# Kernel tuning notes

Measured on AMD Instinct MI355X. Metric: run time of the kernel, lower is better.

Reference implementation:

```python
import jax, jax.numpy as jnp
import numpy as np

EPS = 1e-07
NUM_ITERATIONS = 3

B, O, H, W, I, D = 8, 32, 14, 14, 32, 16


def squash(s, axis=-1):
    # squared norm over capsule dim
    sq = jnp.sum(s * s, axis=axis)                      # [..., ] norms
    safe = jnp.sqrt(sq + EPS)
    factor = sq / (1.0 + sq)
    return (factor / safe)[..., None] * s


def setup_inputs() -> dict:
    key = jax.random.key(0)
    k1, = jax.random.split(key, 1)
    preds = jax.random.normal(k1, (B, O, H, W, I, D), dtype=jnp.float32)
    b = jnp.zeros((1, O, H, W, I), dtype=jnp.float32)   # routing logits param
    return {"tensor_of_prediction_vector": preds, "b": b}


def reference(tensor_of_prediction_vector, b):
    preds = tensor_of_prediction_vector                 # [B,O,H,W,I,D]
    c = jax.nn.softmax(b, axis=-1)                      # [1,O,H,W,I]
    v = squash(jnp.sum(c[..., None] * preds, axis=-2))  # [B,O,H,W,D]
    b_batch = b
    for _ in range(NUM_ITERATIONS):
        # agreement: dot(pred, v) over capsule dim -> [B,O,H,W,I]
        b_batch = b_batch + jnp.sum(preds * v[..., None, :], axis=-1)
        c = jax.nn.softmax(b_batch, axis=-1)
        v = squash(jnp.sum(preds * c[..., None], axis=-2))
    return v
```

## Files before the change

kernel.cpp:

```cpp
#include <hip/hip_runtime.h>


#define EPSQ 1e-7f

constexpr int NI = 32, ND = 16;
constexpr int SITES = 50176;
constexpr int OHW   = 6272;
constexpr int THREADS = 256;
constexpr int BLOCKS  = SITES / 64;

__device__ __forceinline__ float dpp_xor1(float x) {
    return __int_as_float(__builtin_amdgcn_mov_dpp(__float_as_int(x), 0xB1, 0xF, 0xF, true));
}
__device__ __forceinline__ float dpp_xor2(float x) {
    return __int_as_float(__builtin_amdgcn_mov_dpp(__float_as_int(x), 0x4E, 0xF, 0xF, true));
}
__device__ __forceinline__ void fma4(float4& a, float c, const float4& x) {
    a.x = fmaf(c, x.x, a.x); a.y = fmaf(c, x.y, a.y);
    a.z = fmaf(c, x.z, a.z); a.w = fmaf(c, x.w, a.w);
}
__device__ __forceinline__ float dot4(const float4& a, const float4& b) {
    return fmaf(a.x, b.x, fmaf(a.y, b.y, fmaf(a.z, b.z, a.w * b.w)));
}
__device__ __forceinline__ void qred4(float4& a) {
    a.x += dpp_xor1(a.x); a.y += dpp_xor1(a.y);
    a.z += dpp_xor1(a.z); a.w += dpp_xor1(a.w);
    a.x += dpp_xor2(a.x); a.y += dpp_xor2(a.y);
    a.z += dpp_xor2(a.z); a.w += dpp_xor2(a.w);
}

__global__ __launch_bounds__(256, 2) void routing_kernel(
    const float* __restrict__ preds,
    const float* __restrict__ bparam,
    float* __restrict__ out)
{
    __shared__ float4 lds4[4096];
    const int tid  = threadIdx.x;
    const int lane = tid & 63;
    const int wib  = tid >> 6;
    const int wave = blockIdx.x * 4 + wib;
    const int q    = lane & 3;
    const int s_w  = lane >> 2;
    const int site = wave * 16 + s_w;

    float4* wlds = lds4 + wib * 1024;
    const float4* pg = (const float4*)preds + (size_t)wave * 2048;

    float4 t0[16], t1[16];
    #pragma unroll
    for (int k = 0; k < 16; ++k) t0[k] = pg[k * 64 + lane];
    #pragma unroll
    for (int k = 0; k < 16; ++k) t1[k] = pg[1024 + k * 64 + lane];

    const int sohw = site % OHW;
    const float4* bb4 = (const float4*)(bparam + (size_t)sohw * NI + q * 8);
    const float4 bA = bb4[0], bB = bb4[1];
    float bl[8] = {bA.x, bA.y, bA.z, bA.w, bB.x, bB.y, bB.z, bB.w};

    float4 p[8][4];
    const int cb = 32 * q;

    #pragma unroll
    for (int k = 0; k < 16; ++k) {
        const int x = k >> 1;
        wlds[x * 128 + ((((k & 1) * 64) + lane) ^ x)] = t0[k];
    }
    asm volatile("s_waitcnt lgkmcnt(0)" ::: "memory");
    if (s_w < 8) {
        const int x = s_w;
        #pragma unroll
        for (int r = 0; r < 8; ++r)
            #pragma unroll
            for (int u = 0; u < 4; ++u)
                p[r][u] = wlds[x * 128 + ((cb + 4 * r + u) ^ x)];
    }
    asm volatile("s_waitcnt lgkmcnt(0)" ::: "memory");
    #pragma unroll
    for (int k = 0; k < 16; ++k) {
        const int x = k >> 1;
        wlds[x * 128 + ((((k & 1) * 64) + lane) ^ x)] = t1[k];
    }
    asm volatile("s_waitcnt lgkmcnt(0)" ::: "memory");
    if (s_w >= 8) {
        const int x = s_w - 8;
        #pragma unroll
        for (int r = 0; r < 8; ++r)
            #pragma unroll
            for (int u = 0; u < 4; ++u)
                p[r][u] = wlds[x * 128 + ((cb + 4 * r + u) ^ x)];
    }

    float4 v0, v1, v2, v3;

    auto pass = [&]() {
        float e[8];
        float sm = 0.0f;
        #pragma unroll
        for (int k = 0; k < 8; ++k) { e[k] = __expf(bl[k]); sm += e[k]; }
        sm += dpp_xor1(sm);
        sm += dpp_xor2(sm);
        const float r = __frcp_rn(sm);

        float4 s0 = {0,0,0,0}, s1 = {0,0,0,0}, s2 = {0,0,0,0}, s3 = {0,0,0,0};
        #pragma unroll
        for (int k = 0; k < 8; ++k) {
            fma4(s0, e[k], p[k][0]); fma4(s1, e[k], p[k][1]);
            fma4(s2, e[k], p[k][2]); fma4(s3, e[k], p[k][3]);
        }
        qred4(s0); qred4(s1); qred4(s2); qred4(s3);

        const float sqt = dot4(s0, s0) + dot4(s1, s1) + dot4(s2, s2) + dot4(s3, s3);
        const float sq  = r * r * sqt;
        const float f   = sq * __frcp_rn(1.0f + sq) * __frsqrt_rn(sq + EPSQ) * r;
        v0.x = f*s0.x; v0.y = f*s0.y; v0.z = f*s0.z; v0.w = f*s0.w;
        v1.x = f*s1.x; v1.y = f*s1.y; v1.z = f*s1.z; v1.w = f*s1.w;
        v2.x = f*s2.x; v2.y = f*s2.y; v2.z = f*s2.z; v2.w = f*s2.w;
        v3.x = f*s3.x; v3.y = f*s3.y; v3.z = f*s3.z; v3.w = f*s3.w;
    };

    pass();

    #pragma unroll
    for (int it = 0; it < 3; ++it) {
        #pragma unroll
        for (int k = 0; k < 8; ++k) {
            bl[k] += dot4(p[k][0], v0) + dot4(p[k][1], v1)
                   + dot4(p[k][2], v2) + dot4(p[k][3], v3);
        }
        pass();
    }

    float4 w = (q == 0) ? v0 : (q == 1) ? v1 : (q == 2) ? v2 : v3;
    ((float4*)out)[(size_t)site * 4 + q] = w;
}

extern "C" void kernel_launch(void* const* d_in, const int* in_sizes, int n_in,
                              void* d_out, int out_size, void* d_ws, size_t ws_size,
                              hipStream_t stream) {
    const float* preds  = (const float*)d_in[0];
    const float* bparam = (const float*)d_in[1];
    float* out = (float*)d_out;
    routing_kernel<<<BLOCKS, THREADS, 0, stream>>>(preds, bparam, out);
}
```

Baseline: 27.64 us.

## Split each site across eight lanes to cut registers and raise occupancy

Result: slower. 32.50 us (+17.6%).

```diff
diff --git a/kernel.cpp b/kernel.cpp
--- a/kernel.cpp
+++ b/kernel.cpp
@@ -2,18 +2,25 @@
 
 
 #define EPSQ 1e-7f
+#define LOG2E 1.442695041f
 
 constexpr int NI = 32, ND = 16;
 constexpr int SITES = 50176;
 constexpr int OHW   = 6272;
 constexpr int THREADS = 256;
-constexpr int BLOCKS  = SITES / 64;
+constexpr int BLOCKS  = SITES / 32;
 
-__device__ __forceinline__ float dpp_xor1(float x) {
+__device__ __forceinline__ float dpp1(float x) {
     return __int_as_float(__builtin_amdgcn_mov_dpp(__float_as_int(x), 0xB1, 0xF, 0xF, true));
 }
-__device__ __forceinline__ float dpp_xor2(float x) {
+__device__ __forceinline__ float dpp2(float x) {
     return __int_as_float(__builtin_amdgcn_mov_dpp(__float_as_int(x), 0x4E, 0xF, 0xF, true));
+}
+__device__ __forceinline__ float dpp4(float x) {
+    return __int_as_float(__builtin_amdgcn_mov_dpp(__float_as_int(x), 0x141, 0xF, 0xF, true));
+}
+__device__ __forceinline__ float red8(float x) {
+    x += dpp1(x); x += dpp2(x); x += dpp4(x); return x;
 }
 __device__ __forceinline__ void fma4(float4& a, float c, const float4& x) {
     a.x = fmaf(c, x.x, a.x); a.y = fmaf(c, x.y, a.y);
@@ -22,116 +29,118 @@
 __device__ __forceinline__ float dot4(const float4& a, const float4& b) {
     return fmaf(a.x, b.x, fmaf(a.y, b.y, fmaf(a.z, b.z, a.w * b.w)));
 }
-__device__ __forceinline__ void qred4(float4& a) {
-    a.x += dpp_xor1(a.x); a.y += dpp_xor1(a.y);
-    a.z += dpp_xor1(a.z); a.w += dpp_xor1(a.w);
-    a.x += dpp_xor2(a.x); a.y += dpp_xor2(a.y);
-    a.z += dpp_xor2(a.z); a.w += dpp_xor2(a.w);
+__device__ __forceinline__ void red8_4(float4& a) {
+    a.x += dpp1(a.x); a.y += dpp1(a.y); a.z += dpp1(a.z); a.w += dpp1(a.w);
+    a.x += dpp2(a.x); a.y += dpp2(a.y); a.z += dpp2(a.z); a.w += dpp2(a.w);
+    a.x += dpp4(a.x); a.y += dpp4(a.y); a.z += dpp4(a.z); a.w += dpp4(a.w);
 }
 
-__global__ __launch_bounds__(256, 2) void routing_kernel(
+__global__ __launch_bounds__(256, 4) void routing_kernel(
     const float* __restrict__ preds,
     const float* __restrict__ bparam,
     float* __restrict__ out)
 {
-    __shared__ float4 lds4[4096];
+    __shared__ float4 lds4[2048];
     const int tid  = threadIdx.x;
     const int lane = tid & 63;
     const int wib  = tid >> 6;
     const int wave = blockIdx.x * 4 + wib;
-    const int q    = lane & 3;
-    const int s_w  = lane >> 2;
-    const int site = wave * 16 + s_w;
+    const int g    = lane & 7;
+    const int s_w  = lane >> 3;
+    const int site = wave * 8 + s_w;
 
-    float4* wlds = lds4 + wib * 1024;
-    const float4* pg = (const float4*)preds + (size_t)wave * 2048;
-
-    float4 t0[16], t1[16];
-    #pragma unroll
-    for (int k = 0; k < 16; ++k) t0[k] = pg[k * 64 + lane];
-    #pragma unroll
-    for (int k = 0; k < 16; ++k) t1[k] = pg[1024 + k * 64 + lane];
+    float4* wlds = lds4 + wib * 512;
+    const float4* pg = (const float4*)preds + (size_t)wave * 1024;
 
     const int sohw = site % OHW;
-    const float4* bb4 = (const float4*)(bparam + (size_t)sohw * NI + q * 8);
-    const float4 bA = bb4[0], bB = bb4[1];
-    float bl[8] = {bA.x, bA.y, bA.z, bA.w, bB.x, bB.y, bB.z, bB.w};
+    const float4 bv = ((const float4*)bparam)[(size_t)sohw * 8 + g];
 
-    float4 p[8][4];
-    const int cb = 32 * q;
+    float4 ta[8], tb[8];
+    #pragma unroll
+    for (int j = 0; j < 8; ++j) ta[j] = pg[j * 64 + lane];
+    #pragma unroll
+    for (int j = 0; j < 8; ++j) tb[j] = pg[512 + j * 64 + lane];
 
-    #pragma unroll
-    for (int k = 0; k < 16; ++k) {
-        const int x = k >> 1;
-        wlds[x * 128 + ((((k & 1) * 64) + lane) ^ x)] = t0[k];
+    auto write_phase = [&](int ph, const float4* t) {
+        #pragma unroll
+        for (int j = 0; j < 8; ++j) {
+            const int x = j >> 1;
+            const int k = ph * 4 + x;
+            const int m = (j & 1) * 64 + lane;
+            wlds[x * 128 + (m ^ k ^ (((j & 1) << 2)))] = t[j];
+        }
+    };
+
+    float4 p[4][4];
+    const int rkey = s_w ^ (g & 4);
+    const int rbase = (s_w & 3) * 128 + 16 * g;
+
+    write_phase(0, ta);
+    asm volatile("s_waitcnt lgkmcnt(0)" ::: "memory");
+    if (s_w < 4) {
+        #pragma unroll
+        for (int r = 0; r < 4; ++r)
+            #pragma unroll
+            for (int u = 0; u < 4; ++u)
+                p[r][u] = wlds[(s_w & 3) * 128 + ((16 * g + 4 * r + u) ^ rkey)];
     }
     asm volatile("s_waitcnt lgkmcnt(0)" ::: "memory");
-    if (s_w < 8) {
-        const int x = s_w;
+    write_phase(1, tb);
+    asm volatile("s_waitcnt lgkmcnt(0)" ::: "memory");
+    if (s_w >= 4) {
         #pragma unroll
-        for (int r = 0; r < 8; ++r)
+        for (int r = 0; r < 4; ++r)
             #pragma unroll
             for (int u = 0; u < 4; ++u)
-                p[r][u] = wlds[x * 128 + ((cb + 4 * r + u) ^ x)];
-    }
-    asm volatile("s_waitcnt lgkmcnt(0)" ::: "memory");
-    #pragma unroll
-    for (int k = 0; k < 16; ++k) {
-        const int x = k >> 1;
-        wlds[x * 128 + ((((k & 1) * 64) + lane) ^ x)] = t1[k];
-    }
-    asm volatile("s_waitcnt lgkmcnt(0)" ::: "memory");
-    if (s_w >= 8) {
-        const int x = s_w - 8;
-        #pragma unroll
-        for (int r = 0; r < 8; ++r)
-            #pragma unroll
-            for (int u = 0; u < 4; ++u)
-                p[r][u] = wlds[x * 128 + ((cb + 4 * r + u) ^ x)];
+                p[r][u] = wlds[(s_w & 3) * 128 + ((16 * g + 4 * r + u) ^ rkey)];
     }
 
-    float4 v0, v1, v2, v3;
+    float bl[4] = {bv.x * LOG2E, bv.y * LOG2E, bv.z * LOG2E, bv.w * LOG2E};
+
+    float4 s0, s1, s2, s3;
+    float  f;
 
     auto pass = [&]() {
-        float e[8];
+        float e[4];
         float sm = 0.0f;
         #pragma unroll
-        for (int k = 0; k < 8; ++k) { e[k] = __expf(bl[k]); sm += e[k]; }
-        sm += dpp_xor1(sm);
-        sm += dpp_xor2(sm);
+        for (int k = 0; k < 4; ++k) { e[k] = __builtin_amdgcn_exp2f(bl[k]); sm += e[k]; }
+        sm = red8(sm);
         const float r = __frcp_rn(sm);
 
-        float4 s0 = {0,0,0,0}, s1 = {0,0,0,0}, s2 = {0,0,0,0}, s3 = {0,0,0,0};
+        s0 = make_float4(0,0,0,0); s1 = make_float4(0,0,0,0);
+        s2 = make_float4(0,0,0,0); s3 = make_float4(0,0,0,0);
         #pragma unroll
-        for (int k = 0; k < 8; ++k) {
+        for (int k = 0; k < 4; ++k) {
             fma4(s0, e[k], p[k][0]); fma4(s1, e[k], p[k][1]);
             fma4(s2, e[k], p[k][2]); fma4(s3, e[k], p[k][3]);
         }
-        qred4(s0); qred4(s1); qred4(s2); qred4(s3);
+        red8_4(s0); red8_4(s1); red8_4(s2); red8_4(s3);
 
         const float sqt = dot4(s0, s0) + dot4(s1, s1) + dot4(s2, s2) + dot4(s3, s3);
         const float sq  = r * r * sqt;
-        const float f   = sq * __frcp_rn(1.0f + sq) * __frsqrt_rn(sq + EPSQ) * r;
-        v0.x = f*s0.x; v0.y = f*s0.y; v0.z = f*s0.z; v0.w = f*s0.w;
-        v1.x = f*s1.x; v1.y = f*s1.y; v1.z = f*s1.z; v1.w = f*s1.w;
-        v2.x = f*s2.x; v2.y = f*s2.y; v2.z = f*s2.z; v2.w = f*s2.w;
-        v3.x = f*s3.x; v3.y = f*s3.y; v3.z = f*s3.z; v3.w = f*s3.w;
+        f = sq * __frcp_rn(1.0f + sq) * __frsqrt_rn(sq + EPSQ) * r;
     };
 
     pass();
 
     #pragma unroll
     for (int it = 0; it < 3; ++it) {
+        const float fl = f * LOG2E;
         #pragma unroll
-        for (int k = 0; k < 8; ++k) {
-            bl[k] += dot4(p[k][0], v0) + dot4(p[k][1], v1)
-                   + dot4(p[k][2], v2) + dot4(p[k][3], v3);
+        for (int k = 0; k < 4; ++k) {
+            const float qk = dot4(p[k][0], s0) + dot4(p[k][1], s1)
+                           + dot4(p[k][2], s2) + dot4(p[k][3], s3);
+            bl[k] = fmaf(fl, qk, bl[k]);
         }
         pass();
     }
 
-    float4 w = (q == 0) ? v0 : (q == 1) ? v1 : (q == 2) ? v2 : v3;
-    ((float4*)out)[(size_t)site * 4 + q] = w;
+    if (g < 4) {
+        float4 w = (g == 0) ? s0 : (g == 1) ? s1 : (g == 2) ? s2 : s3;
+        w.x *= f; w.y *= f; w.z *= f; w.w *= f;
+        ((float4*)out)[(size_t)site * 4 + g] = w;
+    }
 }
 
 extern "C" void kernel_launch(void* const* d_in, const int* in_sizes, int n_in,
```
